# Performance work log

Hardware: AMD Instinct MI355X
Metric: run time of the kernel (lower is better)

The kernel has to match this reference:

```python
import jax, jax.numpy as jnp
import numpy as np

N_NODES = 100000
FEAT_DIM = 128
EMBED_DIM = 128
NUM_SAMPLE = 10


def setup_inputs() -> dict:
    key = jax.random.key(0)
    k1, k2, k3, k4, k5 = jax.random.split(key, 5)
    features = jax.random.normal(k1, (N_NODES, FEAT_DIM), dtype=jnp.float32)
    W1 = jax.random.normal(k2, (EMBED_DIM, FEAT_DIM), dtype=jnp.float32) * (1.0 / np.sqrt(FEAT_DIM))
    W2 = jax.random.normal(k3, (EMBED_DIM, EMBED_DIM), dtype=jnp.float32) * (1.0 / np.sqrt(EMBED_DIM))
    adj = jax.random.randint(k4, (N_NODES, NUM_SAMPLE), 0, N_NODES, dtype=jnp.int64)
    nodes = jax.random.randint(k5, (N_NODES,), 0, N_NODES, dtype=jnp.int64)
    return {"features": features, "W1": W1, "W2": W2, "adj": adj, "nodes": nodes}


def reference(features, W1, W2, adj, nodes):
    # 2-layer GraphSAGE with gcn=True: mean over {self} U sampled neighbors,
    # then relu(agg @ W.T). Layer 1 is computed for all nodes since layer 2
    # needs embeddings of arbitrary neighbors.
    n = features.shape[0]
    self_idx = jnp.arange(n, dtype=adj.dtype)[:, None]            # [N,1]
    neigh1 = jnp.concatenate([self_idx, adj], axis=1)             # [N,S+1]
    agg1 = jnp.mean(features[neigh1], axis=1)                     # [N,F] (gather+mean)
    h1 = jax.nn.relu(agg1 @ W1.T)                                 # [N,E]

    neigh2 = jnp.concatenate([nodes[:, None], adj[nodes]], axis=1)  # [B,S+1]
    agg2 = jnp.mean(h1[neigh2], axis=1)                           # [B,E]
    out = jax.nn.relu(agg2 @ W2.T).T                              # [E,B], Encoder returns embed_dim x num_nodes
    return out
```

## Files before the change

kernel.cpp:

```cpp
#include <hip/hip_runtime.h>

#define N_NODES 100000
#define DIM 128
#define NS 10
#define SCALE (1.0f / 11.0f)

typedef unsigned int uint;
typedef unsigned short ushort;
typedef __attribute__((ext_vector_type(8))) short bf16x8;
typedef __attribute__((ext_vector_type(4))) float f32x4;

__device__ inline float bl(uint u) {
    union { uint x; float f; } c; c.x = u << 16; return c.f;
}
__device__ inline uint f2b(float x) {
    union { float f; uint u; } c; c.f = x;
    return (c.u + 0x7FFFu + ((c.u >> 16) & 1u)) >> 16;
}

__global__ __launch_bounds__(256) void wsplit(const float* __restrict__ W1,
                                              const float* __restrict__ W2,
                                              ushort* __restrict__ o) {
    const int i = blockIdx.x * 256 + threadIdx.x;
    const float a = W1[i];
    uint h = f2b(a);
    o[i] = (ushort)h;
    o[16384 + i] = (ushort)f2b(a - bl(h));
    const float b = W2[i];
    h = f2b(b);
    o[32768 + i] = (ushort)h;
    o[49152 + i] = (ushort)f2b(b - bl(h));
}

__global__ __launch_bounds__(256, 2) void gemm1(const float* __restrict__ X,
                                                const ushort* __restrict__ Whi,
                                                const ushort* __restrict__ Wlo,
                                                ushort* __restrict__ C) {
    __shared__ __align__(16) ushort lds[8192];
    const int t = threadIdx.x;
    const int lane = t & 63;
    const int wave = t >> 6;
    const int m16 = lane & 15;
    const int kq = lane >> 4;
    const int r0 = blockIdx.x * 32;

    const int v0 = t, v1 = t + 256;
    const int ln0 = v0 & 63, ln1 = v1 & 63;
    const float* s0 = X + (size_t)(r0 + (v0 >> 8) * 16 + (ln0 & 15)) * DIM +
                      ((v0 >> 6) & 3) * 32 + (ln0 >> 4) * 8;
    const float* s1 = X + (size_t)(r0 + (v1 >> 8) * 16 + (ln1 & 15)) * DIM +
                      ((v1 >> 6) & 3) * 32 + (ln1 >> 4) * 8;
    const float4 f00 = *(const float4*)(s0);
    const float4 f01 = *(const float4*)(s0 + 4);
    const float4 f10 = *(const float4*)(s1);
    const float4 f11 = *(const float4*)(s1 + 4);

    bf16x8 wh[2][4], wl[2][4];
#pragma unroll
    for (int c = 0; c < 2; ++c)
#pragma unroll
        for (int ks = 0; ks < 4; ++ks) {
            const size_t off = (size_t)((2 * wave + c) * 16 + m16) * DIM + ks * 32 + kq * 8;
            wh[c][ks] = *(const bf16x8*)(Whi + off);
            wl[c][ks] = *(const bf16x8*)(Wlo + off);
        }

    {
        const float xs[8] = {f00.x, f00.y, f00.z, f00.w, f01.x, f01.y, f01.z, f01.w};
        bf16x8 hi, lo;
#pragma unroll
        for (int j = 0; j < 8; ++j) {
            const uint hb = f2b(xs[j]);
            hi[j] = (short)hb;
            lo[j] = (short)f2b(xs[j] - bl(hb));
        }
        *(bf16x8*)(lds + (v0 >> 6) * 512 + ln0 * 8) = hi;
        *(bf16x8*)(lds + 4096 + (v0 >> 6) * 512 + ln0 * 8) = lo;
    }
    {
        const float xs[8] = {f10.x, f10.y, f10.z, f10.w, f11.x, f11.y, f11.z, f11.w};
        bf16x8 hi, lo;
#pragma unroll
        for (int j = 0; j < 8; ++j) {
            const uint hb = f2b(xs[j]);
            hi[j] = (short)hb;
            lo[j] = (short)f2b(xs[j] - bl(hb));
        }
        *(bf16x8*)(lds + (v1 >> 6) * 512 + ln1 * 8) = hi;
        *(bf16x8*)(lds + 4096 + (v1 >> 6) * 512 + ln1 * 8) = lo;
    }
    __syncthreads();

    f32x4 acc[2][2];
#pragma unroll
    for (int bt = 0; bt < 2; ++bt)
#pragma unroll
        for (int c = 0; c < 2; ++c) acc[bt][c] = (f32x4){0.f, 0.f, 0.f, 0.f};

#pragma unroll
    for (int ks = 0; ks < 4; ++ks) {
#pragma unroll
        for (int bt = 0; bt < 2; ++bt) {
            const int g = bt * 4 + ks;
            const bf16x8 xh = *(const bf16x8*)(lds + g * 512 + lane * 8);
            const bf16x8 xl = *(const bf16x8*)(lds + 4096 + g * 512 + lane * 8);
#pragma unroll
            for (int c = 0; c < 2; ++c) {
                acc[bt][c] = __builtin_amdgcn_mfma_f32_16x16x32_bf16(wh[c][ks], xh, acc[bt][c], 0, 0, 0);
                acc[bt][c] = __builtin_amdgcn_mfma_f32_16x16x32_bf16(wl[c][ks], xh, acc[bt][c], 0, 0, 0);
                acc[bt][c] = __builtin_amdgcn_mfma_f32_16x16x32_bf16(wh[c][ks], xl, acc[bt][c], 0, 0, 0);
            }
        }
    }

#pragma unroll
    for (int bt = 0; bt < 2; ++bt) {
        const size_t row = (size_t)(r0 + bt * 16 + m16);
#pragma unroll
        for (int c = 0; c < 2; ++c) {
            uint2 w;
            w.x = f2b(acc[bt][c][0]) | (f2b(acc[bt][c][1]) << 16);
            w.y = f2b(acc[bt][c][2]) | (f2b(acc[bt][c][3]) << 16);
            *(uint2*)(C + row * DIM + (2 * wave + c) * 16 + kq * 4) = w;
        }
    }
}

__global__ __launch_bounds__(256) void agg1(const ushort* __restrict__ FW,
                                            const int* __restrict__ adj,
                                            ushort* __restrict__ H) {
    __shared__ int idx_lds[320];
    const int t = threadIdx.x;
    const int r0 = blockIdx.x * 32;
    for (int l = t; l < 320; l += 256)
        idx_lds[l] = adj[(size_t)r0 * NS + l];
    __syncthreads();
    const int team = t >> 4;
    const int j = t & 15;
#pragma unroll
    for (int rp = 0; rp < 2; ++rp) {
        const int ri = team * 2 + rp;
        const int row = r0 + ri;
        uint4 u[11];
        u[0] = *(const uint4*)(FW + (size_t)row * DIM + j * 8);
#pragma unroll
        for (int s = 0; s < NS; ++s)
            u[1 + s] = *(const uint4*)(FW + (size_t)idx_lds[ri * NS + s] * DIM + j * 8);
        float a[8];
#pragma unroll
        for (int k = 0; k < 8; ++k) a[k] = 0.f;
#pragma unroll
        for (int s = 0; s < 11; ++s) {
            a[0] += bl(u[s].x); a[1] += bl(u[s].x >> 16);
            a[2] += bl(u[s].y); a[3] += bl(u[s].y >> 16);
            a[4] += bl(u[s].z); a[5] += bl(u[s].z >> 16);
            a[6] += bl(u[s].w); a[7] += bl(u[s].w >> 16);
        }
        uint4 w;
        w.x = f2b(fmaxf(a[0] * SCALE, 0.f)) | (f2b(fmaxf(a[1] * SCALE, 0.f)) << 16);
        w.y = f2b(fmaxf(a[2] * SCALE, 0.f)) | (f2b(fmaxf(a[3] * SCALE, 0.f)) << 16);
        w.z = f2b(fmaxf(a[4] * SCALE, 0.f)) | (f2b(fmaxf(a[5] * SCALE, 0.f)) << 16);
        w.w = f2b(fmaxf(a[6] * SCALE, 0.f)) | (f2b(fmaxf(a[7] * SCALE, 0.f)) << 16);
        *(uint4*)(H + (size_t)row * DIM + j * 8) = w;
    }
}

__global__ __launch_bounds__(256, 2) void gemm2f(const ushort* __restrict__ H,
                                                 const int* __restrict__ adj,
                                                 const int* __restrict__ nodes,
                                                 const ushort* __restrict__ Whi,
                                                 const ushort* __restrict__ Wlo,
                                                 float* __restrict__ out) {
    __shared__ __align__(16) ushort plds[4096];
    __shared__ int idx_lds[32 * 11];
    const int t = threadIdx.x;
    const int lane = t & 63;
    const int wave = t >> 6;
    const int m16w = lane & 15;
    const int kq = lane >> 4;
    const int r0 = blockIdx.x * 32;

    if (t < 32) idx_lds[t * 11] = nodes[r0 + t];

    bf16x8 wh[2][4], wl[2][4];
#pragma unroll
    for (int c = 0; c < 2; ++c)
#pragma unroll
        for (int ks = 0; ks < 4; ++ks) {
            const size_t off = (size_t)((2 * wave + c) * 16 + m16w) * DIM + ks * 32 + kq * 8;
            wh[c][ks] = *(const bf16x8*)(Whi + off);
            wl[c][ks] = *(const bf16x8*)(Wlo + off);
        }
    __syncthreads();
    for (int l = t; l < 320; l += 256) {
        const int bi = l / 10;
        const int s = l - bi * 10;
        idx_lds[bi * 11 + 1 + s] = adj[(size_t)idx_lds[bi * 11] * NS + s];
    }
    __syncthreads();

    const int team = t >> 4;
    const int j = t & 15;
#pragma unroll
    for (int rp = 0; rp < 2; ++rp) {
        const int ri = team * 2 + rp;
        uint4 u[11];
#pragma unroll
        for (int s = 0; s < 11; ++s)
            u[s] = *(const uint4*)(H + (size_t)idx_lds[ri * 11 + s] * DIM + j * 8);
        float a[8];
#pragma unroll
        for (int k = 0; k < 8; ++k) a[k] = 0.f;
#pragma unroll
        for (int s = 0; s < 11; ++s) {
            a[0] += bl(u[s].x); a[1] += bl(u[s].x >> 16);
            a[2] += bl(u[s].y); a[3] += bl(u[s].y >> 16);
            a[4] += bl(u[s].z); a[5] += bl(u[s].z >> 16);
            a[6] += bl(u[s].w); a[7] += bl(u[s].w >> 16);
        }
        bf16x8 pw;
#pragma unroll
        for (int k = 0; k < 8; ++k) pw[k] = (short)f2b(a[k] * SCALE);
        const int bt = ri >> 4;
        const int m16 = ri & 15;
        *(bf16x8*)(plds + (bt * 4 + (j >> 2)) * 512 + ((j & 3) * 16 + m16) * 8) = pw;
    }
    __syncthreads();

    f32x4 acc[2][2];
#pragma unroll
    for (int bt = 0; bt < 2; ++bt)
#pragma unroll
        for (int c = 0; c < 2; ++c) acc[bt][c] = (f32x4){0.f, 0.f, 0.f, 0.f};

#pragma unroll
    for (int ks = 0; ks < 4; ++ks) {
#pragma unroll
        for (int bt = 0; bt < 2; ++bt) {
            const bf16x8 pa = *(const bf16x8*)(plds + (bt * 4 + ks) * 512 + lane * 8);
#pragma unroll
            for (int c = 0; c < 2; ++c) {
                acc[bt][c] = __builtin_amdgcn_mfma_f32_16x16x32_bf16(pa, wh[c][ks], acc[bt][c], 0, 0, 0);
                acc[bt][c] = __builtin_amdgcn_mfma_f32_16x16x32_bf16(pa, wl[c][ks], acc[bt][c], 0, 0, 0);
            }
        }
    }

#pragma unroll
    for (int bt = 0; bt < 2; ++bt) {
        const int b = r0 + bt * 16 + kq * 4;
#pragma unroll
        for (int c = 0; c < 2; ++c) {
            const int e = (2 * wave + c) * 16 + m16w;
            float4 v;
            v.x = fmaxf(acc[bt][c][0], 0.f);
            v.y = fmaxf(acc[bt][c][1], 0.f);
            v.z = fmaxf(acc[bt][c][2], 0.f);
            v.w = fmaxf(acc[bt][c][3], 0.f);
            *(float4*)(out + (size_t)e * N_NODES + b) = v;
        }
    }
}

extern "C" void kernel_launch(void* const* d_in, const int* in_sizes, int n_in,
                              void* d_out, int out_size, void* d_ws, size_t ws_size,
                              hipStream_t stream) {
    const float* features = (const float*)d_in[0];
    const float* W1 = (const float*)d_in[1];
    const float* W2 = (const float*)d_in[2];
    const int* adj = (const int*)d_in[3];
    const int* nodes = (const int*)d_in[4];
    float* out = (float*)d_out;

    const size_t NE = (size_t)N_NODES * DIM;
    ushort* fw = (ushort*)d_ws;
    ushort* h1 = fw + NE;
    ushort* wpl = h1 + NE;
    ushort* w1hi = wpl;
    ushort* w1lo = wpl + 16384;
    ushort* w2hi = wpl + 32768;
    ushort* w2lo = wpl + 49152;

    wsplit<<<64, 256, 0, stream>>>(W1, W2, wpl);
    gemm1<<<N_NODES / 32, 256, 0, stream>>>(features, w1hi, w1lo, fw);
    agg1<<<N_NODES / 32, 256, 0, stream>>>(fw, adj, h1);
    gemm2f<<<N_NODES / 32, 256, 0, stream>>>(h1, adj, nodes, w2hi, w2lo, out);
}
```

Baseline: 144.9 us.

## Split fused layer-2 gather+GEMM into separate aggregation and GEMM kernels

```diff
diff --git a/kernel.cpp b/kernel.cpp
--- a/kernel.cpp
+++ b/kernel.cpp
@@ -165,32 +165,14 @@
     }
 }
 
-__global__ __launch_bounds__(256, 2) void gemm2f(const ushort* __restrict__ H,
-                                                 const int* __restrict__ adj,
-                                                 const int* __restrict__ nodes,
-                                                 const ushort* __restrict__ Whi,
-                                                 const ushort* __restrict__ Wlo,
-                                                 float* __restrict__ out) {
-    __shared__ __align__(16) ushort plds[4096];
+__global__ __launch_bounds__(256) void agg2b(const ushort* __restrict__ H,
+                                             const int* __restrict__ adj,
+                                             const int* __restrict__ nodes,
+                                             ushort* __restrict__ P) {
     __shared__ int idx_lds[32 * 11];
     const int t = threadIdx.x;
-    const int lane = t & 63;
-    const int wave = t >> 6;
-    const int m16w = lane & 15;
-    const int kq = lane >> 4;
     const int r0 = blockIdx.x * 32;
-
     if (t < 32) idx_lds[t * 11] = nodes[r0 + t];
-
-    bf16x8 wh[2][4], wl[2][4];
-#pragma unroll
-    for (int c = 0; c < 2; ++c)
-#pragma unroll
-        for (int ks = 0; ks < 4; ++ks) {
-            const size_t off = (size_t)((2 * wave + c) * 16 + m16w) * DIM + ks * 32 + kq * 8;
-            wh[c][ks] = *(const bf16x8*)(Whi + off);
-            wl[c][ks] = *(const bf16x8*)(Wlo + off);
-        }
     __syncthreads();
     for (int l = t; l < 320; l += 256) {
         const int bi = l / 10;
@@ -198,7 +180,6 @@
         idx_lds[bi * 11 + 1 + s] = adj[(size_t)idx_lds[bi * 11] * NS + s];
     }
     __syncthreads();
-
     const int team = t >> 4;
     const int j = t & 15;
 #pragma unroll
@@ -218,13 +199,48 @@
             a[4] += bl(u[s].z); a[5] += bl(u[s].z >> 16);
             a[6] += bl(u[s].w); a[7] += bl(u[s].w >> 16);
         }
-        bf16x8 pw;
-#pragma unroll
-        for (int k = 0; k < 8; ++k) pw[k] = (short)f2b(a[k] * SCALE);
-        const int bt = ri >> 4;
-        const int m16 = ri & 15;
-        *(bf16x8*)(plds + (bt * 4 + (j >> 2)) * 512 + ((j & 3) * 16 + m16) * 8) = pw;
-    }
+        uint4 w;
+        w.x = f2b(a[0] * SCALE) | (f2b(a[1] * SCALE) << 16);
+        w.y = f2b(a[2] * SCALE) | (f2b(a[3] * SCALE) << 16);
+        w.z = f2b(a[4] * SCALE) | (f2b(a[5] * SCALE) << 16);
+        w.w = f2b(a[6] * SCALE) | (f2b(a[7] * SCALE) << 16);
+        *(uint4*)(P + (size_t)(r0 + ri) * DIM + j * 8) = w;
+    }
+}
+
+__global__ __launch_bounds__(256, 2) void gemm2t(const ushort* __restrict__ P,
+                                                 const ushort* __restrict__ Whi,
+                                                 const ushort* __restrict__ Wlo,
+                                                 float* __restrict__ out) {
+    __shared__ __align__(16) ushort lds[4096];
+    const int t = threadIdx.x;
+    const int lane = t & 63;
+    const int wave = t >> 6;
+    const int m16 = lane & 15;
+    const int kq = lane >> 4;
+    const int r0 = blockIdx.x * 32;
+
+    const int v0 = t, v1 = t + 256;
+    const int ln0 = v0 & 63, ln1 = v1 & 63;
+    const ushort* s0 = P + (size_t)(r0 + (v0 >> 8) * 16 + (ln0 & 15)) * DIM +
+                       ((v0 >> 6) & 3) * 32 + (ln0 >> 4) * 8;
+    const ushort* s1 = P + (size_t)(r0 + (v1 >> 8) * 16 + (ln1 & 15)) * DIM +
+                       ((v1 >> 6) & 3) * 32 + (ln1 >> 4) * 8;
+    const bf16x8 p0 = *(const bf16x8*)(s0);
+    const bf16x8 p1 = *(const bf16x8*)(s1);
+
+    bf16x8 wh[2][4], wl[2][4];
+#pragma unroll
+    for (int c = 0; c < 2; ++c)
+#pragma unroll
+        for (int ks = 0; ks < 4; ++ks) {
+            const size_t off = (size_t)((2 * wave + c) * 16 + m16) * DIM + ks * 32 + kq * 8;
+            wh[c][ks] = *(const bf16x8*)(Whi + off);
+            wl[c][ks] = *(const bf16x8*)(Wlo + off);
+        }
+
+    *(bf16x8*)(lds + (v0 >> 6) * 512 + ln0 * 8) = p0;
+    *(bf16x8*)(lds + (v1 >> 6) * 512 + ln1 * 8) = p1;
     __syncthreads();
 
     f32x4 acc[2][2];
@@ -237,7 +253,7 @@
     for (int ks = 0; ks < 4; ++ks) {
 #pragma unroll
         for (int bt = 0; bt < 2; ++bt) {
-            const bf16x8 pa = *(const bf16x8*)(plds + (bt * 4 + ks) * 512 + lane * 8);
+            const bf16x8 pa = *(const bf16x8*)(lds + (bt * 4 + ks) * 512 + lane * 8);
 #pragma unroll
             for (int c = 0; c < 2; ++c) {
                 acc[bt][c] = __builtin_amdgcn_mfma_f32_16x16x32_bf16(pa, wh[c][ks], acc[bt][c], 0, 0, 0);
@@ -251,7 +267,7 @@
         const int b = r0 + bt * 16 + kq * 4;
 #pragma unroll
         for (int c = 0; c < 2; ++c) {
-            const int e = (2 * wave + c) * 16 + m16w;
+            const int e = (2 * wave + c) * 16 + m16;
             float4 v;
             v.x = fmaxf(acc[bt][c][0], 0.f);
             v.y = fmaxf(acc[bt][c][1], 0.f);
@@ -284,5 +300,6 @@
     wsplit<<<64, 256, 0, stream>>>(W1, W2, wpl);
     gemm1<<<N_NODES / 32, 256, 0, stream>>>(features, w1hi, w1lo, fw);
     agg1<<<N_NODES / 32, 256, 0, stream>>>(fw, adj, h1);
-    gemm2f<<<N_NODES / 32, 256, 0, stream>>>(h1, adj, nodes, w2hi, w2lo, out);
-}
+    agg2b<<<N_NODES / 32, 256, 0, stream>>>(h1, adj, nodes, fw);
+    gemm2t<<<N_NODES / 32, 256, 0, stream>>>(fw, w2hi, w2lo, out);
+}
```

Result: slower. 155.1 us (+7.0%).
